# Kernel optimization log

Measured on AMD Instinct MI355X. Metric: run time of the kernel, lower is better.

## Reference

```python
import jax, jax.numpy as jnp
import numpy as np
from jax import lax

N_CLASS, EMB, HID, NUM_LAYER = 32000, 256, 512, 2
BATCH, SEQ = 128, 512


def setup_inputs() -> dict:
    key = jax.random.key(0)
    ks = jax.random.split(key, 8)
    s = 0.05
    return {
        "X": jax.random.randint(ks[0], (BATCH, SEQ), 0, N_CLASS),
        "C": jax.random.normal(ks[1], (N_CLASS, EMB), jnp.float32) * s,
        "W_ax": jax.random.normal(ks[2], (HID, EMB), jnp.float32) * s,
        "W_aa": jax.random.normal(ks[3], (HID, HID), jnp.float32) * s,   # shared across all layers ([m]*n quirk)
        "W_aa_l": jax.random.normal(ks[4], (HID, HID), jnp.float32) * s, # shared inter-layer weight
        "b_a": jnp.ones((HID,), jnp.float32),                            # shared bias
        "W_out": jax.random.normal(ks[5], (N_CLASS, HID), jnp.float32) * s,
        "b_out": jnp.ones((N_CLASS,), jnp.float32),
    }


def reference(X, C, W_ax, W_aa, W_aa_l, b_a, W_out, b_out):
    emb = C[X]                       # [B, T, E]
    xs = jnp.swapaxes(emb, 0, 1)     # [T, B, E] time-major
    B = X.shape[0]

    def step(m, x):                  # m: [L, B, H]
        h0 = jnp.tanh(x @ W_ax.T + m[0] @ W_aa.T + b_a)
        hs = [h0]
        for l in range(1, NUM_LAYER):
            hs.append(jnp.tanh(hs[l - 1] @ W_aa_l.T + m[l] @ W_aa.T + b_a))
        return jnp.stack(hs), None

    m0 = jnp.zeros((NUM_LAYER, B, HID), emb.dtype)
    m_final, _ = lax.scan(step, m0, xs)
    return m_final[NUM_LAYER - 1] @ W_out.T + b_out  # [B, n_class]
```

## Files before the change

### kernel.cpp

```cpp
#include <hip/hip_runtime.h>
#include <hip/hip_bf16.h>
#include <stdint.h>


#define VOCAB 32000
#define EMB   256
#define HID   512
#define BATCH 128
#define SEQ   512
#define SLOT  8192
#define NSLOT 4

typedef __attribute__((ext_vector_type(8))) short bf16x8;
typedef __attribute__((ext_vector_type(4))) float f32x4;

__device__ inline short f2bf(float f) {
  union { float f; uint32_t u; } v; v.f = f;
  uint32_t u = v.u;
  uint32_t r = (u + 0x7FFFu + ((u >> 16) & 1u)) >> 16;
  return (short)r;
}
__device__ inline float bf2f(unsigned short s) {
  union { uint32_t u; float f; } v; v.u = ((uint32_t)s) << 16;
  return v.f;
}
__device__ inline bf16x8 cvt8(f32x4 x0, f32x4 x1) {
  bf16x8 r;
  r[0]=f2bf(x0[0]); r[1]=f2bf(x0[1]); r[2]=f2bf(x0[2]); r[3]=f2bf(x0[3]);
  r[4]=f2bf(x1[0]); r[5]=f2bf(x1[1]); r[6]=f2bf(x1[2]); r[7]=f2bf(x1[3]);
  return r;
}
__device__ inline f32x4 mfma16(bf16x8 a, bf16x8 b, f32x4 c) {
  return __builtin_amdgcn_mfma_f32_16x16x32_bf16(a, b, c, 0, 0, 0);
}
__device__ inline float fast_tanh(float x) {
  x = fminf(30.f, fmaxf(-30.f, x));
  float e = __expf(2.f * x);
  return (e - 1.f) * __builtin_amdgcn_rcpf(e + 1.f);
}

#define VMCNT0  asm volatile("s_waitcnt vmcnt(0)" ::: "memory")
#define VMCNT16 asm volatile("s_waitcnt vmcnt(16)" ::: "memory")
#define LGKM0   asm volatile("s_waitcnt lgkmcnt(0)" ::: "memory")
#define SCHED0  __builtin_amdgcn_sched_barrier(0)

__device__ inline void st16(unsigned short* p, bf16x8 v) {
  asm volatile("global_store_dwordx4 %0, %1, off sc0 sc1" :: "v"(p), "v"(v) : "memory");
}
__device__ inline void sig(unsigned* p, unsigned v) {
  asm volatile("global_store_dword %0, %1, off sc0 sc1" :: "v"(p), "v"(v) : "memory");
}
__device__ inline void poll2(const unsigned* f0, const unsigned* f1,
                             unsigned t0, unsigned t1) {
  const int lane = threadIdx.x & 63;
  bool ok = (lane >= 32);
  const unsigned* fp = (lane < 16) ? (f0 + lane) : (f1 + (lane - 16));
  const unsigned tgt = (lane < 16) ? t0 : t1;
  unsigned v = 0; int guard = 0;
  while (true) {
    if (!ok) {
      asm volatile("global_load_dword %0, %1, off sc0 sc1\n\ts_waitcnt vmcnt(0)"
                   : "=v"(v) : "v"(fp) : "memory");
      ok = (v >= tgt);
    }
    if (__ballot(ok) == ~0ull) break;
    __builtin_amdgcn_s_sleep(1);
    if (++guard > 30000) break;
  }
}

__global__ void k_init(unsigned* __restrict__ p, int n) {
  int i = blockIdx.x * 256 + threadIdx.x;
  if (i < n) p[i] = 0u;
}

__global__ void __launch_bounds__(256) k_cw(const float* __restrict__ C,
                                            const float* __restrict__ Wax,
                                            unsigned short* __restrict__ CW) {
  const int tid = threadIdx.x, lane = tid & 63, wv = tid >> 6;
  const int l15 = lane & 15, l4 = lane >> 4;
  const int row = blockIdx.x * 64 + wv * 16 + l15;
  bf16x8 a[8];
  const float* crow = C + (size_t)row * EMB;
#pragma unroll
  for (int s = 0; s < 8; ++s) {
    const f32x4* p = (const f32x4*)(crow + s * 32 + l4 * 8);
    a[s] = cvt8(p[0], p[1]);
  }
  const int row_o_base = blockIdx.x * 64 + wv * 16 + l4 * 4;
  for (int ct = 0; ct < 8; ++ct) {
    f32x4 acc[4];
#pragma unroll
    for (int nf = 0; nf < 4; ++nf) acc[nf] = (f32x4){0.f, 0.f, 0.f, 0.f};
#pragma unroll
    for (int s = 0; s < 8; ++s) {
#pragma unroll
      for (int nf = 0; nf < 4; ++nf) {
        int col = ct * 64 + nf * 16 + l15;
        const f32x4* bp = (const f32x4*)(Wax + (size_t)col * EMB + s * 32 + l4 * 8);
        bf16x8 b = cvt8(bp[0], bp[1]);
        acc[nf] = mfma16(a[s], b, acc[nf]);
      }
    }
#pragma unroll
    for (int nf = 0; nf < 4; ++nf) {
      int col = ct * 64 + nf * 16 + l15;
#pragma unroll
      for (int r = 0; r < 4; ++r)
        CW[(size_t)(row_o_base + r) * HID + col] = (unsigned short)f2bf(acc[nf][r]);
    }
  }
}

__global__ void __launch_bounds__(256, 1) k_scan(
    const int* __restrict__ X, const float* __restrict__ Waa, const float* __restrict__ Wal,
    const float* __restrict__ ba, const unsigned short* __restrict__ CW,
    unsigned short* __restrict__ h0buf, unsigned short* __restrict__ h1buf,
    unsigned* __restrict__ flags) {
  extern __shared__ unsigned short lds[];
  unsigned short* ldsWaa = lds;
  unsigned short* ldsWal = lds + 64 * 512;
  unsigned short* packb  = lds + 2 * 64 * 512;
  const int tid = threadIdx.x, lane = tid & 63, wv = tid >> 6;
  const int l15 = lane & 15, l4 = lane >> 4;
  const int g = blockIdx.x & 7, mem = blockIdx.x >> 3;
  const int colslice = mem * 64;
  unsigned* fl = flags + g * 64;
  unsigned* f0 = fl;
  unsigned* f1 = fl + 16;

  for (int c = tid; c < 64 * 64; c += 256) {
    int row = c >> 6, u = c & 63, us = u ^ (row & 7);
    {
      const f32x4* p = (const f32x4*)(Waa + (size_t)(colslice + row) * HID + u * 8);
      *(bf16x8*)(ldsWaa + row * 512 + us * 8) = cvt8(p[0], p[1]);
    }
    {
      const f32x4* p = (const f32x4*)(Wal + (size_t)(colslice + row) * HID + u * 8);
      *(bf16x8*)(ldsWal + row * 512 + us * 8) = cvt8(p[0], p[1]);
    }
  }

  const int cb  = (wv & 1) * 2;
  const int jc0 = colslice + cb * 16 + l15;
  const int jc1 = jc0 + 16;
  const float ba0 = ba[jc0], ba1 = ba[jc1];
  const int wb0 = (cb * 16 + l15) * 512;
  const int wb1 = wb0 + 16 * 512;
  const int swz = l15 & 7;
  const int aoff = l4 * 128 + l15 * 8;
  unsigned short* pk = packb + wv * 512;
  const int pl0 = ((l15 >> 3) + 0) * 128 + (l4 * 4) * 8 + (l15 & 7);
  const int pl1 = ((l15 >> 3) + 2) * 128 + (l4 * 4) * 8 + (l15 & 7);
  const int stbase = mem * 1024 + cb * 256 + lane * 8;
  const int brow = g * 16 + l4 * 4;
  unsigned short* h0g = h0buf + (size_t)g * (NSLOT * SLOT);
  unsigned short* h1g = h1buf + (size_t)g * (NSLOT * SLOT);
  __syncthreads();

#define WFRAG(W, wb, s) (*(const bf16x8*)((W) + (wb) + ((((s) * 4 + l4) ^ swz) * 8)))
#define LOAD16(arr, base)                                                         \
  _Pragma("unroll") for (int s = 0; s < 16; ++s)                                  \
    asm volatile("global_load_dwordx4 %0, %1, off sc0 sc1"                        \
                 : "=v"(arr[s]) : "v"((base) + s * 1024) : "memory");

  if (wv < 2) {
    unsigned* myf = f0 + 2 * mem + (wv & 1);
    int idxA[4];
    unsigned cw0[4], cw1[4];
    {
      int id0[4];
#pragma unroll
      for (int r = 0; r < 4; ++r)
        asm volatile("global_load_dword %0, %1, off"
                     : "=v"(id0[r]) : "v"(X + (size_t)(brow + r) * SEQ) : "memory");
      VMCNT0;
#pragma unroll
      for (int r = 0; r < 4; ++r) {
        const unsigned short* c0 = CW + (size_t)id0[r] * HID + jc0;
        asm volatile("global_load_ushort %0, %1, off" : "=v"(cw0[r]) : "v"(c0) : "memory");
        asm volatile("global_load_ushort %0, %1, off" : "=v"(cw1[r]) : "v"(c0 + 16) : "memory");
      }
#pragma unroll
      for (int r = 0; r < 4; ++r)
        asm volatile("global_load_dword %0, %1, off"
                     : "=v"(idxA[r]) : "v"(X + (size_t)(brow + r) * SEQ + 1) : "memory");
    }
    for (int t = 0; t < SEQ; ++t) {
      poll2(f0, f1, (unsigned)t, (unsigned)(t >= 2 ? t - 2 : 0));
      bf16x8 a0[16];
      const char* pa0 = (const char*)(h0g + ((t + 3) & 3) * SLOT + aoff);
      LOAD16(a0, pa0)
      VMCNT0; SCHED0;
      f32x4 acc0 = (f32x4){0.f, 0.f, 0.f, 0.f};
      f32x4 acc1 = (f32x4){0.f, 0.f, 0.f, 0.f};
#pragma unroll
      for (int s = 0; s < 16; ++s) {
        bf16x8 a = a0[s];
        acc0 = mfma16(a, WFRAG(ldsWaa, wb0, s), acc0);
        acc1 = mfma16(a, WFRAG(ldsWaa, wb1, s), acc1);
      }
#pragma unroll
      for (int r = 0; r < 4; ++r) {
        float v0 = fast_tanh(acc0[r] + bf2f((unsigned short)cw0[r]) + ba0);
        float v1 = fast_tanh(acc1[r] + bf2f((unsigned short)cw1[r]) + ba1);
        pk[pl0 + r * 8] = (unsigned short)f2bf(v0);
        pk[pl1 + r * 8] = (unsigned short)f2bf(v1);
      }
      LGKM0; SCHED0;
      bf16x8 ov = *(const bf16x8*)(pk + lane * 8);
      st16(h0g + (t & 3) * SLOT + stbase, ov);
      VMCNT0;
      if (lane == 0) sig(myf, (unsigned)(t + 1));
#pragma unroll
      for (int r = 0; r < 4; ++r) {
        const unsigned short* c0 = CW + (size_t)idxA[r] * HID + jc0;
        asm volatile("global_load_ushort %0, %1, off" : "=v"(cw0[r]) : "v"(c0) : "memory");
        asm volatile("global_load_ushort %0, %1, off" : "=v"(cw1[r]) : "v"(c0 + 16) : "memory");
      }
      const int tp = (t + 2 < SEQ) ? t + 2 : SEQ - 1;
#pragma unroll
      for (int r = 0; r < 4; ++r)
        asm volatile("global_load_dword %0, %1, off"
                     : "=v"(idxA[r]) : "v"(X + (size_t)(brow + r) * SEQ + tp) : "memory");
    }
  } else {
    unsigned* myf = f1 + 2 * mem + (wv & 1);
    for (int t = 0; t <= SEQ; ++t) {
      poll2(f0, f1, (unsigned)t, (unsigned)t);
      if (t >= 1) {
        bf16x8 a1[16], a2[16];
        const char* pa1 = (const char*)(h0g + ((t + 3) & 3) * SLOT + aoff);
        const char* pa2 = (const char*)(h1g + ((t + 2) & 3) * SLOT + aoff);
        LOAD16(a1, pa1)
        LOAD16(a2, pa2)
        VMCNT16; SCHED0;
        f32x4 acc0 = (f32x4){0.f, 0.f, 0.f, 0.f};
        f32x4 acc1 = (f32x4){0.f, 0.f, 0.f, 0.f};
#pragma unroll
        for (int s = 0; s < 16; ++s) {
          bf16x8 a = a1[s];
          acc0 = mfma16(a, WFRAG(ldsWal, wb0, s), acc0);
          acc1 = mfma16(a, WFRAG(ldsWal, wb1, s), acc1);
        }
        VMCNT0; SCHED0;
#pragma unroll
        for (int s = 0; s < 16; ++s) {
          bf16x8 a = a2[s];
          acc0 = mfma16(a, WFRAG(ldsWaa, wb0, s), acc0);
          acc1 = mfma16(a, WFRAG(ldsWaa, wb1, s), acc1);
        }
#pragma unroll
        for (int r = 0; r < 4; ++r) {
          float v0 = fast_tanh(acc0[r] + ba0);
          float v1 = fast_tanh(acc1[r] + ba1);
          pk[pl0 + r * 8] = (unsigned short)f2bf(v0);
          pk[pl1 + r * 8] = (unsigned short)f2bf(v1);
        }
        LGKM0; SCHED0;
        bf16x8 ov = *(const bf16x8*)(pk + lane * 8);
        st16(h1g + ((t + 3) & 3) * SLOT + stbase, ov);
        VMCNT0;
      }
      if (lane == 0) sig(myf, (unsigned)(t + 1));
    }
  }
#undef LOAD16
#undef WFRAG
}

__global__ void __launch_bounds__(256) k_out(const float* __restrict__ Wout,
                                             const float* __restrict__ bout,
                                             const unsigned short* __restrict__ h1buf,
                                             float* __restrict__ out) {
  const int tid = threadIdx.x, lane = tid & 63, wv = tid >> 6;
  const int l15 = lane & 15, l4 = lane >> 4;
  const int col = blockIdx.x * 64 + wv * 16 + l15;
  const float bo = bout[col];
  f32x4 acc[8];
#pragma unroll
  for (int rt = 0; rt < 8; ++rt) acc[rt] = (f32x4){0.f, 0.f, 0.f, 0.f};
  const int aoff = l4 * 128 + l15 * 8;
#pragma unroll 4
  for (int s = 0; s < 16; ++s) {
    const f32x4* bp = (const f32x4*)(Wout + (size_t)col * HID + s * 32 + l4 * 8);
    bf16x8 b = cvt8(bp[0], bp[1]);
#pragma unroll
    for (int rt = 0; rt < 8; ++rt) {
      const unsigned short* ap = h1buf + (size_t)rt * (NSLOT * SLOT) + 3 * SLOT + aoff + s * 512;
      acc[rt] = mfma16(*(const bf16x8*)ap, b, acc[rt]);
    }
  }
#pragma unroll
  for (int rt = 0; rt < 8; ++rt) {
#pragma unroll
    for (int r = 0; r < 4; ++r) {
      int row = rt * 16 + l4 * 4 + r;
      out[(size_t)row * VOCAB + col] = acc[rt][r] + bo;
    }
  }
}

extern "C" void kernel_launch(void* const* d_in, const int* in_sizes, int n_in,
                              void* d_out, int out_size, void* d_ws, size_t ws_size,
                              hipStream_t stream) {
  const int*   X    = (const int*)d_in[0];
  const float* C    = (const float*)d_in[1];
  const float* Wax  = (const float*)d_in[2];
  const float* Waa  = (const float*)d_in[3];
  const float* Wal  = (const float*)d_in[4];
  const float* ba   = (const float*)d_in[5];
  const float* Wout = (const float*)d_in[6];
  const float* bout = (const float*)d_in[7];
  float* out = (float*)d_out;
  char* ws = (char*)d_ws;
  (void)in_sizes; (void)n_in; (void)out_size;

  const size_t cw_bytes = (size_t)VOCAB * HID * 2;
  const size_t h_bytes  = 8ull * NSLOT * SLOT * 2;
  const size_t off_h0 = cw_bytes;
  const size_t off_h1 = off_h0 + h_bytes;
  const size_t off_fl = off_h1 + h_bytes;
  const size_t fl_bytes = 8 * 64 * 4;
  if (ws_size < off_fl + fl_bytes) return;

  unsigned short* CWp = (unsigned short*)(ws);
  unsigned short* h0  = (unsigned short*)(ws + off_h0);
  unsigned short* h1  = (unsigned short*)(ws + off_h1);
  unsigned*       fl  = (unsigned*)(ws + off_fl);

  const int zero_words = (int)((2 * h_bytes + fl_bytes) / 4);
  hipLaunchKernelGGL(k_init, dim3((zero_words + 255) / 256), dim3(256), 0, stream,
                     (unsigned*)(ws + off_h0), zero_words);
  hipLaunchKernelGGL(k_cw, dim3(VOCAB / 64), dim3(256), 0, stream, C, Wax, CWp);
  hipFuncSetAttribute((const void*)k_scan, hipFuncAttributeMaxDynamicSharedMemorySize, 135168);
  hipLaunchKernelGGL(k_scan, dim3(64), dim3(256), 135168, stream,
                     X, Waa, Wal, ba, CWp, h0, h1, fl);
  hipLaunchKernelGGL(k_out, dim3(VOCAB / 64), dim3(256), 0, stream, Wout, bout, h1, out);
}
```

Before: 2.040 ms.

## Probe cache coherence at runtime and use lighter cache bits for inter-block exchange

Each group of 8 blocks first runs a handshake test that checks whether stores with only sc0 and loads with nt are seen by the other blocks in the group. If every member passes, the scan uses these weaker-scope stores and loads for hidden-state exchange and flag polling; otherwise it keeps the sc0 sc1 system-scope path. The poll loop also drops its s_sleep so it spins tighter. The aim is to cut the latency of each per-step cross-block exchange, at the cost of a startup handshake and of relying on a coherence behaviour the hardware does not guarantee.

```diff
diff --git a/kernel.cpp b/kernel.cpp
--- a/kernel.cpp
+++ b/kernel.cpp
@@ -44,27 +44,45 @@
 #define LGKM0   asm volatile("s_waitcnt lgkmcnt(0)" ::: "memory")
 #define SCHED0  __builtin_amdgcn_sched_barrier(0)
 
-__device__ inline void st16(unsigned short* p, bf16x8 v) {
-  asm volatile("global_store_dwordx4 %0, %1, off sc0 sc1" :: "v"(p), "v"(v) : "memory");
-}
-__device__ inline void sig(unsigned* p, unsigned v) {
-  asm volatile("global_store_dword %0, %1, off sc0 sc1" :: "v"(p), "v"(v) : "memory");
-}
+template <bool FAST>
+__device__ inline void stq(unsigned short* p, bf16x8 v) {
+  if (FAST) asm volatile("global_store_dwordx4 %0, %1, off sc0"     :: "v"(p), "v"(v) : "memory");
+  else      asm volatile("global_store_dwordx4 %0, %1, off sc0 sc1" :: "v"(p), "v"(v) : "memory");
+}
+template <bool FAST>
+__device__ inline void sigst(unsigned* p, unsigned v) {
+  if (FAST) asm volatile("global_store_dword %0, %1, off sc0"     :: "v"(p), "v"(v) : "memory");
+  else      asm volatile("global_store_dword %0, %1, off sc0 sc1" :: "v"(p), "v"(v) : "memory");
+}
+template <bool FAST>
+__device__ inline unsigned ldf(const unsigned* p) {
+  unsigned v;
+  if (FAST) asm volatile("global_load_dword %0, %1, off nt\n\ts_waitcnt vmcnt(0)"
+                         : "=v"(v) : "v"(p) : "memory");
+  else      asm volatile("global_load_dword %0, %1, off sc0 sc1\n\ts_waitcnt vmcnt(0)"
+                         : "=v"(v) : "v"(p) : "memory");
+  return v;
+}
+template <bool FAST>
+__device__ inline void load16(bf16x8* arr, const char* base) {
+#pragma unroll
+  for (int s = 0; s < 16; ++s) {
+    if (FAST) asm volatile("global_load_dwordx4 %0, %1, off nt"
+                           : "=v"(arr[s]) : "v"(base + s * 1024) : "memory");
+    else      asm volatile("global_load_dwordx4 %0, %1, off sc0 sc1"
+                           : "=v"(arr[s]) : "v"(base + s * 1024) : "memory");
+  }
+}
+template <bool FAST>
 __device__ inline void poll2(const unsigned* f0, const unsigned* f1,
                              unsigned t0, unsigned t1) {
   const int lane = threadIdx.x & 63;
   bool ok = (lane >= 32);
   const unsigned* fp = (lane < 16) ? (f0 + lane) : (f1 + (lane - 16));
   const unsigned tgt = (lane < 16) ? t0 : t1;
-  unsigned v = 0; int guard = 0;
-  while (true) {
-    if (!ok) {
-      asm volatile("global_load_dword %0, %1, off sc0 sc1\n\ts_waitcnt vmcnt(0)"
-                   : "=v"(v) : "v"(fp) : "memory");
-      ok = (v >= tgt);
-    }
-    if (__ballot(ok) == ~0ull) break;
-    __builtin_amdgcn_s_sleep(1);
+  int guard = 0;
+  while (__ballot(ok) != ~0ull) {
+    if (!ok) ok = (ldf<FAST>(fp) >= tgt);
     if (++guard > 30000) break;
   }
 }
@@ -110,6 +128,120 @@
         CW[(size_t)(row_o_base + r) * HID + col] = (unsigned short)f2bf(acc[nf][r]);
     }
   }
+}
+
+template <bool FAST>
+__device__ __forceinline__ void scan_run(
+    const int* __restrict__ X, const unsigned short* __restrict__ CW,
+    unsigned short* __restrict__ h0g, unsigned short* __restrict__ h1g,
+    unsigned* __restrict__ f0, unsigned* __restrict__ f1,
+    const unsigned short* ldsWaa, const unsigned short* ldsWal, unsigned short* pk,
+    int jc0, int jc1, float ba0, float ba1, int wb0, int wb1, int swz,
+    int aoff, int pl0, int pl1, int stbase, int brow, int mem, int wv, int lane) {
+  const int l4 = lane >> 4;
+#define WFRAG(W, wb, s) (*(const bf16x8*)((W) + (wb) + ((((s) * 4 + l4) ^ swz) * 8)))
+  if (wv < 2) {
+    unsigned* myf = f0 + 2 * mem + (wv & 1);
+    int idxA[4];
+    unsigned cw0[4], cw1[4];
+    {
+      int id0[4];
+#pragma unroll
+      for (int r = 0; r < 4; ++r)
+        asm volatile("global_load_dword %0, %1, off"
+                     : "=v"(id0[r]) : "v"(X + (size_t)(brow + r) * SEQ) : "memory");
+      VMCNT0;
+#pragma unroll
+      for (int r = 0; r < 4; ++r) {
+        const unsigned short* c0 = CW + (size_t)id0[r] * HID + jc0;
+        asm volatile("global_load_ushort %0, %1, off" : "=v"(cw0[r]) : "v"(c0) : "memory");
+        asm volatile("global_load_ushort %0, %1, off" : "=v"(cw1[r]) : "v"(c0 + 16) : "memory");
+      }
+#pragma unroll
+      for (int r = 0; r < 4; ++r)
+        asm volatile("global_load_dword %0, %1, off"
+                     : "=v"(idxA[r]) : "v"(X + (size_t)(brow + r) * SEQ + 1) : "memory");
+    }
+    for (int t = 0; t < SEQ; ++t) {
+      poll2<FAST>(f0, f1, (unsigned)t, (unsigned)(t >= 2 ? t - 2 : 0));
+      bf16x8 a0[16];
+      const char* pa0 = (const char*)(h0g + ((t + 3) & 3) * SLOT + aoff);
+      load16<FAST>(a0, pa0);
+      VMCNT0; SCHED0;
+      f32x4 acc0 = (f32x4){0.f, 0.f, 0.f, 0.f};
+      f32x4 acc1 = (f32x4){0.f, 0.f, 0.f, 0.f};
+#pragma unroll
+      for (int s = 0; s < 16; ++s) {
+        bf16x8 a = a0[s];
+        acc0 = mfma16(a, WFRAG(ldsWaa, wb0, s), acc0);
+        acc1 = mfma16(a, WFRAG(ldsWaa, wb1, s), acc1);
+      }
+#pragma unroll
+      for (int r = 0; r < 4; ++r) {
+        float v0 = fast_tanh(acc0[r] + bf2f((unsigned short)cw0[r]) + ba0);
+        float v1 = fast_tanh(acc1[r] + bf2f((unsigned short)cw1[r]) + ba1);
+        pk[pl0 + r * 8] = (unsigned short)f2bf(v0);
+        pk[pl1 + r * 8] = (unsigned short)f2bf(v1);
+      }
+      LGKM0; SCHED0;
+      bf16x8 ov = *(const bf16x8*)(pk + lane * 8);
+      stq<FAST>(h0g + (t & 3) * SLOT + stbase, ov);
+      VMCNT0;
+      if (lane == 0) sigst<FAST>(myf, (unsigned)(t + 1));
+#pragma unroll
+      for (int r = 0; r < 4; ++r) {
+        const unsigned short* c0 = CW + (size_t)idxA[r] * HID + jc0;
+        asm volatile("global_load_ushort %0, %1, off" : "=v"(cw0[r]) : "v"(c0) : "memory");
+        asm volatile("global_load_ushort %0, %1, off" : "=v"(cw1[r]) : "v"(c0 + 16) : "memory");
+      }
+      const int tp = (t + 2 < SEQ) ? t + 2 : SEQ - 1;
+#pragma unroll
+      for (int r = 0; r < 4; ++r)
+        asm volatile("global_load_dword %0, %1, off"
+                     : "=v"(idxA[r]) : "v"(X + (size_t)(brow + r) * SEQ + tp) : "memory");
+    }
+  } else {
+    unsigned* myf = f1 + 2 * mem + (wv & 1);
+    for (int t = 0; t <= SEQ; ++t) {
+      poll2<FAST>(f0, f1, (unsigned)t, (unsigned)t);
+      if (t >= 1) {
+        bf16x8 a1[16], a2[16];
+        const char* pa1 = (const char*)(h0g + ((t + 3) & 3) * SLOT + aoff);
+        const char* pa2 = (const char*)(h1g + ((t + 2) & 3) * SLOT + aoff);
+        load16<FAST>(a1, pa1);
+        load16<FAST>(a2, pa2);
+        VMCNT16; SCHED0;
+        f32x4 acc0 = (f32x4){0.f, 0.f, 0.f, 0.f};
+        f32x4 acc1 = (f32x4){0.f, 0.f, 0.f, 0.f};
+#pragma unroll
+        for (int s = 0; s < 16; ++s) {
+          bf16x8 a = a1[s];
+          acc0 = mfma16(a, WFRAG(ldsWal, wb0, s), acc0);
+          acc1 = mfma16(a, WFRAG(ldsWal, wb1, s), acc1);
+        }
+        VMCNT0; SCHED0;
+#pragma unroll
+        for (int s = 0; s < 16; ++s) {
+          bf16x8 a = a2[s];
+          acc0 = mfma16(a, WFRAG(ldsWaa, wb0, s), acc0);
+          acc1 = mfma16(a, WFRAG(ldsWaa, wb1, s), acc1);
+        }
+#pragma unroll
+        for (int r = 0; r < 4; ++r) {
+          float v0 = fast_tanh(acc0[r] + ba0);
+          float v1 = fast_tanh(acc1[r] + ba1);
+          pk[pl0 + r * 8] = (unsigned short)f2bf(v0);
+          pk[pl1 + r * 8] = (unsigned short)f2bf(v1);
+        }
+        LGKM0; SCHED0;
+        bf16x8 ov = *(const bf16x8*)(pk + lane * 8);
+        stq<FAST>(h1g + ((t + 3) & 3) * SLOT + stbase, ov);
+        VMCNT0;
+      }
+      if (lane == 0) sigst<FAST>(myf, (unsigned)(t + 1));
+    }
+  }
+#undef WFRAG
 }
 
 __global__ void __launch_bounds__(256, 1) k_scan(
@@ -121,6 +253,7 @@
   unsigned short* ldsWaa = lds;
   unsigned short* ldsWal = lds + 64 * 512;
   unsigned short* packb  = lds + 2 * 64 * 512;
+  __shared__ unsigned s_mode;
   const int tid = threadIdx.x, lane = tid & 63, wv = tid >> 6;
   const int l15 = lane & 15, l4 = lane >> 4;
   const int g = blockIdx.x & 7, mem = blockIdx.x >> 3;
@@ -128,6 +261,9 @@
   unsigned* fl = flags + g * 64;
   unsigned* f0 = fl;
   unsigned* f1 = fl + 16;
+  unsigned* pp = fl + 32;
+  unsigned* pv = fl + 40;
+  unsigned* pd = flags + 512 + g * 32;
 
   for (int c = tid; c < 64 * 64; c += 256) {
     int row = c >> 6, u = c & 63, us = u ^ (row & 7);
@@ -140,6 +276,46 @@
       *(bf16x8*)(ldsWal + row * 512 + us * 8) = cvt8(p[0], p[1]);
     }
   }
+
+  if (wv == 0) {
+    const unsigned MAG1 = 0x5EED0000u + (unsigned)(g << 8);
+    const unsigned MAG2 = 0x7EED0000u + (unsigned)(g << 8);
+    bool okm = true;
+    if (lane == 0) {
+      asm volatile("global_store_dword %0, %1, off sc0"
+                   :: "v"(pd + mem), "v"(MAG1 + (unsigned)mem) : "memory");
+      VMCNT0;
+      __hip_atomic_store(pp + mem, 1u, __ATOMIC_RELAXED, __HIP_MEMORY_SCOPE_AGENT);
+    }
+    { bool ok = (lane >= 8); int gd = 0;
+      while (__ballot(ok) != ~0ull) {
+        if (!ok) ok = (ldf<false>(pp + (lane & 7)) >= 1u);
+        if (++gd > 500000) break; } }
+    if (lane < 8) okm = (ldf<true>(pd + lane) == MAG1 + (unsigned)lane);
+    if (lane == 0) {
+      asm volatile("global_store_dword %0, %1, off sc0"
+                   :: "v"(pd + mem), "v"(MAG2 + (unsigned)mem) : "memory");
+      VMCNT0;
+      __hip_atomic_store(pp + mem, 2u, __ATOMIC_RELAXED, __HIP_MEMORY_SCOPE_AGENT);
+    }
+    { bool ok = (lane >= 8); int gd = 0;
+      while (__ballot(ok) != ~0ull) {
+        if (!ok) ok = (ldf<false>(pp + (lane & 7)) >= 2u);
+        if (++gd > 500000) break; } }
+    if (lane < 8) okm = okm && (ldf<true>(pd + lane) == MAG2 + (unsigned)lane);
+    bool myv = (__ballot(okm) == ~0ull);
+    if (lane == 0)
+      asm volatile("global_store_dword %0, %1, off sc0 sc1"
+                   :: "v"(pv + mem), "v"(myv ? 1u : 2u) : "memory");
+    { bool ok = (lane >= 8); unsigned vv = 1u; int gd = 0;
+      while (__ballot(ok) != ~0ull) {
+        if (!ok) { vv = ldf<false>(pv + (lane & 7)); ok = (vv != 0u); }
+        if (++gd > 500000) break; }
+      bool f = (lane >= 8) || (vv == 1u);
+      if (lane == 0) s_mode = (__ballot(f) == ~0ull) ? 1u : 0u; }
+  }
+  __syncthreads();
+  const bool fastmode = (s_mode != 0u);
 
   const int cb  = (wv & 1) * 2;
   const int jc0 = colslice + cb * 16 + l15;
@@ -156,117 +332,15 @@
   const int brow = g * 16 + l4 * 4;
   unsigned short* h0g = h0buf + (size_t)g * (NSLOT * SLOT);
   unsigned short* h1g = h1buf + (size_t)g * (NSLOT * SLOT);
-  __syncthreads();
-
-#define WFRAG(W, wb, s) (*(const bf16x8*)((W) + (wb) + ((((s) * 4 + l4) ^ swz) * 8)))
-#define LOAD16(arr, base)                                                         \
-  _Pragma("unroll") for (int s = 0; s < 16; ++s)                                  \
-    asm volatile("global_load_dwordx4 %0, %1, off sc0 sc1"                        \
-                 : "=v"(arr[s]) : "v"((base) + s * 1024) : "memory");
-
-  if (wv < 2) {
-    unsigned* myf = f0 + 2 * mem + (wv & 1);
-    int idxA[4];
-    unsigned cw0[4], cw1[4];
-    {
-      int id0[4];
-#pragma unroll
-      for (int r = 0; r < 4; ++r)
-        asm volatile("global_load_dword %0, %1, off"
-                     : "=v"(id0[r]) : "v"(X + (size_t)(brow + r) * SEQ) : "memory");
-      VMCNT0;
-#pragma unroll
-      for (int r = 0; r < 4; ++r) {
-        const unsigned short* c0 = CW + (size_t)id0[r] * HID + jc0;
-        asm volatile("global_load_ushort %0, %1, off" : "=v"(cw0[r]) : "v"(c0) : "memory");
-        asm volatile("global_load_ushort %0, %1, off" : "=v"(cw1[r]) : "v"(c0 + 16) : "memory");
-      }
-#pragma unroll
-      for (int r = 0; r < 4; ++r)
-        asm volatile("global_load_dword %0, %1, off"
-                     : "=v"(idxA[r]) : "v"(X + (size_t)(brow + r) * SEQ + 1) : "memory");
-    }
-    for (int t = 0; t < SEQ; ++t) {
-      poll2(f0, f1, (unsigned)t, (unsigned)(t >= 2 ? t - 2 : 0));
-      bf16x8 a0[16];
-      const char* pa0 = (const char*)(h0g + ((t + 3) & 3) * SLOT + aoff);
-      LOAD16(a0, pa0)
-      VMCNT0; SCHED0;
-      f32x4 acc0 = (f32x4){0.f, 0.f, 0.f, 0.f};
-      f32x4 acc1 = (f32x4){0.f, 0.f, 0.f, 0.f};
-#pragma unroll
-      for (int s = 0; s < 16; ++s) {
-        bf16x8 a = a0[s];
-        acc0 = mfma16(a, WFRAG(ldsWaa, wb0, s), acc0);
-        acc1 = mfma16(a, WFRAG(ldsWaa, wb1, s), acc1);
-      }
-#pragma unroll
-      for (int r = 0; r < 4; ++r) {
-        float v0 = fast_tanh(acc0[r] + bf2f((unsigned short)cw0[r]) + ba0);
-        float v1 = fast_tanh(acc1[r] + bf2f((unsigned short)cw1[r]) + ba1);
-        pk[pl0 + r * 8] = (unsigned short)f2bf(v0);
-        pk[pl1 + r * 8] = (unsigned short)f2bf(v1);
-      }
-      LGKM0; SCHED0;
-      bf16x8 ov = *(const bf16x8*)(pk + lane * 8);
-      st16(h0g + (t & 3) * SLOT + stbase, ov);
-      VMCNT0;
-      if (lane == 0) sig(myf, (unsigned)(t + 1));
-#pragma unroll
-      for (int r = 0; r < 4; ++r) {
-        const unsigned short* c0 = CW + (size_t)idxA[r] * HID + jc0;
-        asm volatile("global_load_ushort %0, %1, off" : "=v"(cw0[r]) : "v"(c0) : "memory");
-        asm volatile("global_load_ushort %0, %1, off" : "=v"(cw1[r]) : "v"(c0 + 16) : "memory");
-      }
-      const int tp = (t + 2 < SEQ) ? t + 2 : SEQ - 1;
-#pragma unroll
-      for (int r = 0; r < 4; ++r)
-        asm volatile("global_load_dword %0, %1, off"
-                     : "=v"(idxA[r]) : "v"(X + (size_t)(brow + r) * SEQ + tp) : "memory");
-    }
-  } else {
-    unsigned* myf = f1 + 2 * mem + (wv & 1);
-    for (int t = 0; t <= SEQ; ++t) {
-      poll2(f0, f1, (unsigned)t, (unsigned)t);
-      if (t >= 1) {
-        bf16x8 a1[16], a2[16];
-        const char* pa1 = (const char*)(h0g + ((t + 3) & 3) * SLOT + aoff);
-        const char* pa2 = (const char*)(h1g + ((t + 2) & 3) * SLOT + aoff);
-        LOAD16(a1, pa1)
-        LOAD16(a2, pa2)
-        VMCNT16; SCHED0;
-        f32x4 acc0 = (f32x4){0.f, 0.f, 0.f, 0.f};
-        f32x4 acc1 = (f32x4){0.f, 0.f, 0.f, 0.f};
-#pragma unroll
-        for (int s = 0; s < 16; ++s) {
-          bf16x8 a = a1[s];
-          acc0 = mfma16(a, WFRAG(ldsWal, wb0, s), acc0);
-          acc1 = mfma16(a, WFRAG(ldsWal, wb1, s), acc1);
-        }
-        VMCNT0; SCHED0;
-#pragma unroll
-        for (int s = 0; s < 16; ++s) {
-          bf16x8 a = a2[s];
-          acc0 = mfma16(a, WFRAG(ldsWaa, wb0, s), acc0);
-          acc1 = mfma16(a, WFRAG(ldsWaa, wb1, s), acc1);
-        }
-#pragma unroll
-        for (int r = 0; r < 4; ++r) {
-          float v0 = fast_tanh(acc0[r] + ba0);
-          float v1 = fast_tanh(acc1[r] + ba1);
-          pk[pl0 + r * 8] = (unsigned short)f2bf(v0);
-          pk[pl1 + r * 8] = (unsigned short)f2bf(v1);
-        }
-        LGKM0; SCHED0;
-        bf16x8 ov = *(const bf16x8*)(pk + lane * 8);
-        st16(h1g + ((t + 3) & 3) * SLOT + stbase, ov);
-        VMCNT0;
-      }
-      if (lane == 0) sig(myf, (unsigned)(t + 1));
-    }
-  }
-#undef LOAD16
-#undef WFRAG
+
+  if (fastmode)
+    scan_run<true>(X, CW, h0g, h1g, f0, f1, ldsWaa, ldsWal, pk,
+                   jc0, jc1, ba0, ba1, wb0, wb1, swz, aoff, pl0, pl1,
+                   stbase, brow, mem, wv, lane);
+  else
+    scan_run<false>(X, CW, h0g, h1g, f0, f1, ldsWaa, ldsWal, pk,
+                    jc0, jc1, ba0, ba1, wb0, wb1, swz, aoff, pl0, pl1,
+                    stbase, brow, mem, wv, lane);
 }
 
 __global__ void __launch_bounds__(256) k_out(const float* __restrict__ Wout,
@@ -321,7 +395,7 @@
   const size_t off_h0 = cw_bytes;
   const size_t off_h1 = off_h0 + h_bytes;
   const size_t off_fl = off_h1 + h_bytes;
-  const size_t fl_bytes = 8 * 64 * 4;
+  const size_t fl_bytes = 2048 + 1024;
   if (ws_size < off_fl + fl_bytes) return;
 
   unsigned short* CWp = (unsigned short*)(ws);
```

New measurement: 4.061 ms. 1.99x slower.

## Split scan layers into separate workgroups and pipeline flag polling loads

Applied to the files above, without the earlier changes.

The scan kernel now launches 128 workgroups instead of 64. Layer-0 and layer-1 recurrence run in different blocks, and layer-1 work is spread over four waves, each owning a 16-column slice, instead of two waves with 32 columns each. That halves the serial MFMA chain per wave on the layer-1 critical path. Flag polling now keeps four loads in flight, replacing the sleep-and-wait spin, which should cut synchronisation latency per step. The cost is more blocks polling the same flags and more cross-workgroup flags to coordinate, and the kernel depends on all 128 blocks being resident at once.

```diff
diff --git a/kernel.cpp b/kernel.cpp
--- a/kernel.cpp
+++ b/kernel.cpp
@@ -6,13 +6,13 @@
 #define VOCAB 32000
 #define EMB   256
 #define HID   512
-#define BATCH 128
 #define SEQ   512
 #define SLOT  8192
 #define NSLOT 4
 
 typedef __attribute__((ext_vector_type(8))) short bf16x8;
 typedef __attribute__((ext_vector_type(4))) float f32x4;
+typedef __attribute__((ext_vector_type(2))) unsigned u32x2;
 
 __device__ inline short f2bf(float f) {
   union { float f; uint32_t u; } v; v.f = f;
@@ -47,27 +47,47 @@
 __device__ inline void st16(unsigned short* p, bf16x8 v) {
   asm volatile("global_store_dwordx4 %0, %1, off sc0 sc1" :: "v"(p), "v"(v) : "memory");
 }
+__device__ inline void st8(unsigned short* p, u32x2 v) {
+  asm volatile("global_store_dwordx2 %0, %1, off sc0 sc1" :: "v"(p), "v"(v) : "memory");
+}
 __device__ inline void sig(unsigned* p, unsigned v) {
   asm volatile("global_store_dword %0, %1, off sc0 sc1" :: "v"(p), "v"(v) : "memory");
 }
-__device__ inline void poll2(const unsigned* f0, const unsigned* f1,
-                             unsigned t0, unsigned t1) {
+
+__device__ __forceinline__ void pollP(const unsigned* f0, const unsigned* f1,
+                                      unsigned t0, unsigned t1,
+                                      unsigned& s0, unsigned& s1,
+                                      unsigned& s2, unsigned& s3) {
   const int lane = threadIdx.x & 63;
-  bool ok = (lane >= 32);
-  const unsigned* fp = (lane < 16) ? (f0 + lane) : (f1 + (lane - 16));
+  const unsigned* fp = (lane < 16) ? (f0 + lane) : (f1 + ((lane - 16) & 31));
   const unsigned tgt = (lane < 16) ? t0 : t1;
-  unsigned v = 0; int guard = 0;
+  bool ok = (lane >= 48);
+#define FISS(r) asm volatile("global_load_dword %0, %1, off sc0 sc1" \
+                             : "=v"(r) : "v"(fp) : "memory")
+  FISS(s0); FISS(s1); FISS(s2); FISS(s3);
+  int guard = 0;
   while (true) {
-    if (!ok) {
-      asm volatile("global_load_dword %0, %1, off sc0 sc1\n\ts_waitcnt vmcnt(0)"
-                   : "=v"(v) : "v"(fp) : "memory");
-      ok = (v >= tgt);
-    }
+    asm volatile("s_waitcnt vmcnt(3)" ::: "memory"); SCHED0;
+    if (!ok) ok = (s0 >= tgt);
     if (__ballot(ok) == ~0ull) break;
-    __builtin_amdgcn_s_sleep(1);
-    if (++guard > 30000) break;
-  }
-}
+    FISS(s0);
+    asm volatile("s_waitcnt vmcnt(3)" ::: "memory"); SCHED0;
+    if (!ok) ok = (s1 >= tgt);
+    if (__ballot(ok) == ~0ull) break;
+    FISS(s1);
+    asm volatile("s_waitcnt vmcnt(3)" ::: "memory"); SCHED0;
+    if (!ok) ok = (s2 >= tgt);
+    if (__ballot(ok) == ~0ull) break;
+    FISS(s2);
+    asm volatile("s_waitcnt vmcnt(3)" ::: "memory"); SCHED0;
+    if (!ok) ok = (s3 >= tgt);
+    if (__ballot(ok) == ~0ull) break;
+    FISS(s3);
+    if (++guard > 20000) break;
+  }
+#undef FISS
+}
+#define PIN4(a,b,c,d) asm volatile("" :: "v"(a), "v"(b), "v"(c), "v"(d))
 
 __global__ void k_init(unsigned* __restrict__ p, int n) {
   int i = blockIdx.x * 256 + threadIdx.x;
@@ -118,13 +138,15 @@
     unsigned short* __restrict__ h0buf, unsigned short* __restrict__ h1buf,
     unsigned* __restrict__ flags) {
   extern __shared__ unsigned short lds[];
+  const int tid = threadIdx.x, lane = tid & 63, wv = tid >> 6;
+  const int l15 = lane & 15, l4 = lane >> 4;
+  const bool isH1 = (blockIdx.x >= 64);
+  const int bb = isH1 ? ((int)blockIdx.x - 64) : (int)blockIdx.x;
+  const int g = bb & 7, m = bb >> 3;
+  const int colslice = m * 64;
   unsigned short* ldsWaa = lds;
   unsigned short* ldsWal = lds + 64 * 512;
-  unsigned short* packb  = lds + 2 * 64 * 512;
-  const int tid = threadIdx.x, lane = tid & 63, wv = tid >> 6;
-  const int l15 = lane & 15, l4 = lane >> 4;
-  const int g = blockIdx.x & 7, mem = blockIdx.x >> 3;
-  const int colslice = mem * 64;
+  unsigned short* packb  = lds + (isH1 ? 2 * 64 * 512 : 64 * 512);
   unsigned* fl = flags + g * 64;
   unsigned* f0 = fl;
   unsigned* f1 = fl + 16;
@@ -135,28 +157,16 @@
       const f32x4* p = (const f32x4*)(Waa + (size_t)(colslice + row) * HID + u * 8);
       *(bf16x8*)(ldsWaa + row * 512 + us * 8) = cvt8(p[0], p[1]);
     }
-    {
+    if (isH1) {
       const f32x4* p = (const f32x4*)(Wal + (size_t)(colslice + row) * HID + u * 8);
       *(bf16x8*)(ldsWal + row * 512 + us * 8) = cvt8(p[0], p[1]);
     }
   }
-
-  const int cb  = (wv & 1) * 2;
-  const int jc0 = colslice + cb * 16 + l15;
-  const int jc1 = jc0 + 16;
-  const float ba0 = ba[jc0], ba1 = ba[jc1];
-  const int wb0 = (cb * 16 + l15) * 512;
-  const int wb1 = wb0 + 16 * 512;
-  const int swz = l15 & 7;
+  __syncthreads();
+
   const int aoff = l4 * 128 + l15 * 8;
-  unsigned short* pk = packb + wv * 512;
-  const int pl0 = ((l15 >> 3) + 0) * 128 + (l4 * 4) * 8 + (l15 & 7);
-  const int pl1 = ((l15 >> 3) + 2) * 128 + (l4 * 4) * 8 + (l15 & 7);
-  const int stbase = mem * 1024 + cb * 256 + lane * 8;
-  const int brow = g * 16 + l4 * 4;
   unsigned short* h0g = h0buf + (size_t)g * (NSLOT * SLOT);
   unsigned short* h1g = h1buf + (size_t)g * (NSLOT * SLOT);
-  __syncthreads();
 
 #define WFRAG(W, wb, s) (*(const bf16x8*)((W) + (wb) + ((((s) * 4 + l4) ^ swz) * 8)))
 #define LOAD16(arr, base)                                                         \
@@ -164,8 +174,21 @@
     asm volatile("global_load_dwordx4 %0, %1, off sc0 sc1"                        \
                  : "=v"(arr[s]) : "v"((base) + s * 1024) : "memory");
 
-  if (wv < 2) {
-    unsigned* myf = f0 + 2 * mem + (wv & 1);
+  if (!isH1) {
+    if (wv >= 2) return;
+    const int cb  = (wv & 1) * 2;
+    const int jc0 = colslice + cb * 16 + l15;
+    const int jc1 = jc0 + 16;
+    const float ba0 = ba[jc0], ba1 = ba[jc1];
+    const int wb0 = (cb * 16 + l15) * 512;
+    const int wb1 = wb0 + 16 * 512;
+    const int swz = l15 & 7;
+    unsigned short* pk = packb + wv * 512;
+    const int pl0 = ((l15 >> 3) + 0) * 128 + (l4 * 4) * 8 + (l15 & 7);
+    const int pl1 = ((l15 >> 3) + 2) * 128 + (l4 * 4) * 8 + (l15 & 7);
+    const int stbase = m * 1024 + cb * 256 + lane * 8;
+    const int brow = g * 16 + l4 * 4;
+    unsigned* myf = f0 + 2 * m + (wv & 1);
     int idxA[4];
     unsigned cw0[4], cw1[4];
     {
@@ -174,7 +197,7 @@
       for (int r = 0; r < 4; ++r)
         asm volatile("global_load_dword %0, %1, off"
                      : "=v"(id0[r]) : "v"(X + (size_t)(brow + r) * SEQ) : "memory");
-      VMCNT0;
+      VMCNT0; SCHED0;
 #pragma unroll
       for (int r = 0; r < 4; ++r) {
         const unsigned short* c0 = CW + (size_t)id0[r] * HID + jc0;
@@ -187,11 +210,13 @@
                      : "=v"(idxA[r]) : "v"(X + (size_t)(brow + r) * SEQ + 1) : "memory");
     }
     for (int t = 0; t < SEQ; ++t) {
-      poll2(f0, f1, (unsigned)t, (unsigned)(t >= 2 ? t - 2 : 0));
+      unsigned s0, s1, s2, s3;
+      pollP(f0, f1, (unsigned)t, (unsigned)(t >= 2 ? t - 2 : 0), s0, s1, s2, s3);
       bf16x8 a0[16];
       const char* pa0 = (const char*)(h0g + ((t + 3) & 3) * SLOT + aoff);
       LOAD16(a0, pa0)
       VMCNT0; SCHED0;
+      PIN4(s0, s1, s2, s3);
       f32x4 acc0 = (f32x4){0.f, 0.f, 0.f, 0.f};
       f32x4 acc1 = (f32x4){0.f, 0.f, 0.f, 0.f};
 #pragma unroll
@@ -225,44 +250,41 @@
                      : "=v"(idxA[r]) : "v"(X + (size_t)(brow + r) * SEQ + tp) : "memory");
     }
   } else {
-    unsigned* myf = f1 + 2 * mem + (wv & 1);
-    for (int t = 0; t <= SEQ; ++t) {
-      poll2(f0, f1, (unsigned)t, (unsigned)t);
-      if (t >= 1) {
-        bf16x8 a1[16], a2[16];
-        const char* pa1 = (const char*)(h0g + ((t + 3) & 3) * SLOT + aoff);
-        const char* pa2 = (const char*)(h1g + ((t + 2) & 3) * SLOT + aoff);
-        LOAD16(a1, pa1)
-        LOAD16(a2, pa2)
-        VMCNT16; SCHED0;
-        f32x4 acc0 = (f32x4){0.f, 0.f, 0.f, 0.f};
-        f32x4 acc1 = (f32x4){0.f, 0.f, 0.f, 0.f};
-#pragma unroll
-        for (int s = 0; s < 16; ++s) {
-          bf16x8 a = a1[s];
-          acc0 = mfma16(a, WFRAG(ldsWal, wb0, s), acc0);
-          acc1 = mfma16(a, WFRAG(ldsWal, wb1, s), acc1);
-        }
-        VMCNT0; SCHED0;
-#pragma unroll
-        for (int s = 0; s < 16; ++s) {
-          bf16x8 a = a2[s];
-          acc0 = mfma16(a, WFRAG(ldsWaa, wb0, s), acc0);
-          acc1 = mfma16(a, WFRAG(ldsWaa, wb1, s), acc1);
-        }
-#pragma unroll
-        for (int r = 0; r < 4; ++r) {
-          float v0 = fast_tanh(acc0[r] + ba0);
-          float v1 = fast_tanh(acc1[r] + ba1);
-          pk[pl0 + r * 8] = (unsigned short)f2bf(v0);
-          pk[pl1 + r * 8] = (unsigned short)f2bf(v1);
-        }
-        LGKM0; SCHED0;
-        bf16x8 ov = *(const bf16x8*)(pk + lane * 8);
-        st16(h1g + ((t + 3) & 3) * SLOT + stbase, ov);
-        VMCNT0;
-      }
-      if (lane == 0) sig(myf, (unsigned)(t + 1));
+    const int jc  = colslice + wv * 16 + l15;
+    const float bav = ba[jc];
+    const int wb = (wv * 16 + l15) * 512;
+    const int swz = l15 & 7;
+    unsigned short* pk = packb + wv * 256;
+    const int pl = (l15 >> 3) * 128 + (l4 * 4) * 8 + (l15 & 7);
+    const int chunk = m * 2 + (wv >> 1);
+    const int stoffs = chunk * 512 + (wv & 1) * 256 + lane * 4;
+    unsigned* myf = f1 + 4 * m + wv;
+    for (int t = 1; t <= SEQ; ++t) {
+      unsigned s0, s1, s2, s3;
+      pollP(f0, f1, (unsigned)t, (unsigned)(t - 1), s0, s1, s2, s3);
+      bf16x8 a1[16], a2[16];
+      const char* pa1 = (const char*)(h0g + ((t + 3) & 3) * SLOT + aoff);
+      const char* pa2 = (const char*)(h1g + ((t + 2) & 3) * SLOT + aoff);
+      LOAD16(a1, pa1)
+      LOAD16(a2, pa2)
+      VMCNT16; SCHED0;
+      PIN4(s0, s1, s2, s3);
+      f32x4 acc = (f32x4){0.f, 0.f, 0.f, 0.f};
+#pragma unroll
+      for (int s = 0; s < 16; ++s) acc = mfma16(a1[s], WFRAG(ldsWal, wb, s), acc);
+      VMCNT0; SCHED0;
+#pragma unroll
+      for (int s = 0; s < 16; ++s) acc = mfma16(a2[s], WFRAG(ldsWaa, wb, s), acc);
+#pragma unroll
+      for (int r = 0; r < 4; ++r) {
+        float v = fast_tanh(acc[r] + bav);
+        pk[pl + r * 8] = (unsigned short)f2bf(v);
+      }
+      LGKM0; SCHED0;
+      u32x2 ov = *(const u32x2*)(pk + lane * 4);
+      st8(h1g + ((t + 3) & 3) * SLOT + stoffs, ov);
+      VMCNT0;
+      if (lane == 0) sig(myf, (unsigned)t);
     }
   }
 #undef LOAD16
@@ -334,7 +356,7 @@
                      (unsigned*)(ws + off_h0), zero_words);
   hipLaunchKernelGGL(k_cw, dim3(VOCAB / 64), dim3(256), 0, stream, C, Wax, CWp);
   hipFuncSetAttribute((const void*)k_scan, hipFuncAttributeMaxDynamicSharedMemorySize, 135168);
-  hipLaunchKernelGGL(k_scan, dim3(64), dim3(256), 135168, stream,
+  hipLaunchKernelGGL(k_scan, dim3(128), dim3(256), 135168, stream,
                      X, Waa, Wal, ba, CWp, h0, h1, fl);
   hipLaunchKernelGGL(k_out, dim3(VOCAB / 64), dim3(256), 0, stream, Wout, bout, h1, out);
 }
```

Result: slower. 4.433 ms (+117.4%).
